# Performance work log

Measured on AMD Instinct MI355X. Metric: run time of the kernel, lower is better.

The kernel has to match this reference:

```python
import jax, jax.numpy as jnp
import numpy as np

B, H, T, D = 4, 16, 1024, 64
M = H * D  # model_dim = 1024
P = 2 * T - 1  # relative position length


def rel_shift(x):
    # x: (B, H, T, 2T-1) -> (B, H, T, T)
    b, h, t1, p = x.shape
    zero_pad = jnp.zeros((b, h, t1, 1), dtype=x.dtype)
    x_padded = jnp.concatenate([zero_pad, x], axis=-1)        # (B,H,T,2T)
    x_padded = x_padded.reshape(b, h, p + 1, t1)              # (B,H,2T,T)
    x = x_padded[:, :, 1:].reshape(b, h, t1, p)               # (B,H,T,2T-1)
    return x[:, :, :, : p // 2 + 1]                           # (B,H,T,T)


def setup_inputs() -> dict:
    key = jax.random.key(0)
    ks = jax.random.split(key, 7)
    q = jax.random.normal(ks[0], (B, H, T, D), dtype=jnp.float32)
    k = jax.random.normal(ks[1], (B, H, T, D), dtype=jnp.float32)
    v = jax.random.normal(ks[2], (B, H, T, D), dtype=jnp.float32)
    pos_emb = jax.random.normal(ks[3], (1, P, M), dtype=jnp.float32)
    attention_mask = jnp.ones((B, 1, 1, T), dtype=bool)
    # learned params
    W_pos = jax.random.normal(ks[4], (M, M), dtype=jnp.float32) * (M ** -0.5)
    pos_bias_u = jax.random.normal(ks[5], (H, D), dtype=jnp.float32) * 0.02
    pos_bias_v = jax.random.normal(ks[6], (H, D), dtype=jnp.float32) * 0.02
    return {"q": q, "k": k, "v": v, "pos_emb": pos_emb,
            "attention_mask": attention_mask, "W_pos": W_pos,
            "pos_bias_u": pos_bias_u, "pos_bias_v": pos_bias_v}


def reference(q, k, v, pos_emb, attention_mask, W_pos, pos_bias_u, pos_bias_v):
    # q, k, v: (B, H, T, D); pos_emb: (1, P, M)
    q_u = q + pos_bias_u[None, :, None, :]
    q_v = q + pos_bias_v[None, :, None, :]
    # linear_pos (no bias), split heads: (1, H, P, D)
    p = (pos_emb @ W_pos.T).reshape(pos_emb.shape[0], -1, H, D).transpose(0, 2, 1, 3)
    matrix_ac = jnp.einsum('bhqd,bhkd->bhqk', q_u, k)          # (B,H,T,T)
    matrix_bd = jnp.einsum('bhqd,hpd->bhqp', q_v, p[0])        # (B,H,T,P)
    matrix_bd = rel_shift(matrix_bd)                           # (B,H,T,T)
    scale = q.shape[-1] ** -0.5
    sim = (matrix_ac + matrix_bd) * scale
    sim = jnp.where(attention_mask, sim, jnp.finfo(sim.dtype).min)
    attn = jax.nn.softmax(sim, axis=-1)
    return jnp.einsum('bhqk,bhkd->bhqd', attn, v)
```

## Files before the change

### kernel.cpp

```cpp
#include <hip/hip_runtime.h>
#include <hip/hip_bf16.h>

#define BB 4
#define HH 16
#define TT 1024
#define DD 64
#define PP 2047
#define MM 1024

typedef __bf16 bf16;
typedef __bf16 bf16x8 __attribute__((ext_vector_type(8)));
typedef float  f32x4  __attribute__((ext_vector_type(4)));

__device__ inline bf16x8 pack8(float4 a, float4 b) {
    bf16x8 r;
    r[0]=(bf16)a.x; r[1]=(bf16)a.y; r[2]=(bf16)a.z; r[3]=(bf16)a.w;
    r[4]=(bf16)b.x; r[5]=(bf16)b.y; r[6]=(bf16)b.z; r[7]=(bf16)b.w;
    return r;
}

__device__ inline bf16x8 pack8_add_scale(float4 a, float4 b, float4 c, float4 d, float s) {
    bf16x8 r;
    r[0]=(bf16)((a.x+c.x)*s); r[1]=(bf16)((a.y+c.y)*s); r[2]=(bf16)((a.z+c.z)*s); r[3]=(bf16)((a.w+c.w)*s);
    r[4]=(bf16)((b.x+d.x)*s); r[5]=(bf16)((b.y+d.y)*s); r[6]=(bf16)((b.z+d.z)*s); r[7]=(bf16)((b.w+d.w)*s);
    return r;
}

__device__ inline unsigned pk2(float a, float b) {
    union { __bf16 h[2]; unsigned u; } x;
    x.h[0] = (__bf16)a; x.h[1] = (__bf16)b;
    return x.u;
}
__device__ inline float lo2f(unsigned u) { return __uint_as_float(u << 16); }
__device__ inline float hi2f(unsigned u) { return __uint_as_float(u & 0xffff0000u); }

__global__ __launch_bounds__(256) void prep_kv_kernel(const float* __restrict__ k,
                                                      const float* __restrict__ v,
                                                      bf16* __restrict__ k_bf,
                                                      bf16* __restrict__ vt) {
    __shared__ __attribute__((aligned(16))) bf16 Tld[64][72];
    const int t = threadIdx.x;
    const int bh = blockIdx.y;
    const int t0 = blockIdx.x * 64;
    const int r = t >> 2, c0 = (t & 3) * 16;
    {
        const float4* src = (const float4*)(k + ((size_t)bh * TT + t0 + r) * DD + c0);
        float4 a = src[0], b = src[1], c = src[2], d = src[3];
        bf16* dst = k_bf + ((size_t)bh * TT + t0 + r) * DD + c0;
        *(bf16x8*)dst       = pack8(a, b);
        *(bf16x8*)(dst + 8) = pack8(c, d);
    }
    {
        const float4* src = (const float4*)(v + ((size_t)bh * TT + t0 + r) * DD + c0);
        float4 a = src[0], b = src[1], c = src[2], d = src[3];
        *(bf16x8*)&Tld[r][c0]     = pack8(a, b);
        *(bf16x8*)&Tld[r][c0 + 8] = pack8(c, d);
    }
    __syncthreads();
    const int dd = t >> 2, j0l = (t & 3) * 16;
    bf16x8 o0, o1;
#pragma unroll
    for (int i = 0; i < 8; ++i) o0[i] = Tld[j0l + i][dd];
#pragma unroll
    for (int i = 0; i < 8; ++i) o1[i] = Tld[j0l + 8 + i][dd];
    bf16* dst = vt + ((size_t)bh * DD + dd) * TT + t0 + j0l;
    *(bf16x8*)dst = o0;
    *(bf16x8*)(dst + 8) = o1;
}

__global__ __launch_bounds__(256) void pos_gemm_kernel(const float* __restrict__ pos_emb,
                                                       const float* __restrict__ W_pos,
                                                       bf16* __restrict__ p_bf) {
    __shared__ __attribute__((aligned(16))) bf16 Abuf[64][72];
    __shared__ __attribute__((aligned(16))) bf16 Bbuf[128][72];
    const int t = threadIdx.x;
    const int w = t >> 6, lane = t & 63, quad = lane >> 4, col = lane & 15;
    const int wr = w >> 1, wc = w & 1;
    const int pp0 = blockIdx.x * 64;
    const int n0 = blockIdx.y * 128;

    f32x4 acc[2][4];
#pragma unroll
    for (int i = 0; i < 2; ++i)
#pragma unroll
        for (int j = 0; j < 4; ++j) acc[i][j] = (f32x4){0.f,0.f,0.f,0.f};

    for (int kt = 0; kt < 16; ++kt) {
        const int k0 = kt * 64;
        __syncthreads();
        {
            const int row = t >> 2, ch = (t & 3) * 16;
            const int pp = pp0 + row;
            if (pp < PP) {
                const float4* s = (const float4*)(pos_emb + (size_t)pp * MM + k0 + ch);
                float4 a = s[0], b = s[1], c = s[2], d = s[3];
                *(bf16x8*)&Abuf[row][ch]     = pack8(a, b);
                *(bf16x8*)&Abuf[row][ch + 8] = pack8(c, d);
            } else {
                float4 z = make_float4(0.f,0.f,0.f,0.f);
                *(bf16x8*)&Abuf[row][ch]     = pack8(z, z);
                *(bf16x8*)&Abuf[row][ch + 8] = pack8(z, z);
            }
        }
#pragma unroll
        for (int c = 0; c < 2; ++c) {
            const int idx = t * 2 + c;
            const int row = idx >> 2, ch = (idx & 3) * 16;
            const float4* s = (const float4*)(W_pos + (size_t)(n0 + row) * MM + k0 + ch);
            float4 a = s[0], b = s[1], cc = s[2], d = s[3];
            *(bf16x8*)&Bbuf[row][ch]     = pack8(a, b);
            *(bf16x8*)&Bbuf[row][ch + 8] = pack8(cc, d);
        }
        __syncthreads();
#pragma unroll
        for (int mt = 0; mt < 2; ++mt) {
            const int ar = wr * 32 + mt * 16 + col;
            const bf16x8 a0 = *(const bf16x8*)&Abuf[ar][quad * 8];
            const bf16x8 a1 = *(const bf16x8*)&Abuf[ar][32 + quad * 8];
#pragma unroll
            for (int nt = 0; nt < 4; ++nt) {
                const int br = wc * 64 + nt * 16 + col;
                const bf16x8 b0 = *(const bf16x8*)&Bbuf[br][quad * 8];
                const bf16x8 b1 = *(const bf16x8*)&Bbuf[br][32 + quad * 8];
                acc[mt][nt] = __builtin_amdgcn_mfma_f32_16x16x32_bf16(a0, b0, acc[mt][nt], 0, 0, 0);
                acc[mt][nt] = __builtin_amdgcn_mfma_f32_16x16x32_bf16(a1, b1, acc[mt][nt], 0, 0, 0);
            }
        }
    }
#pragma unroll
    for (int mt = 0; mt < 2; ++mt)
#pragma unroll
        for (int nt = 0; nt < 4; ++nt)
#pragma unroll
            for (int reg = 0; reg < 4; ++reg) {
                const int pp = pp0 + wr * 32 + mt * 16 + quad * 4 + reg;
                if (pp < PP) {
                    const int n = n0 + wc * 64 + nt * 16 + col;
                    p_bf[((size_t)(n >> 6) * PP + pp) * DD + (n & 63)] = (bf16)acc[mt][nt][reg];
                }
            }
}

__global__ __launch_bounds__(256, 3) void flash_kernel(const float* __restrict__ q,
                                                       const bf16* __restrict__ k_bf,
                                                       const bf16* __restrict__ vt_g,
                                                       const bf16* __restrict__ p_bf,
                                                       const float* __restrict__ bias_u,
                                                       const float* __restrict__ bias_v,
                                                       float* __restrict__ out) {
    __shared__ __attribute__((aligned(16))) bf16 Kld[64][72];
    __shared__ __attribute__((aligned(16))) bf16 Vt[64][72];
    __shared__ __attribute__((aligned(16))) bf16 Sp[4][16][72];
    __shared__ __attribute__((aligned(16))) bf16 Pring[128][72];

    const int t = threadIdx.x;
    const int w = t >> 6, lane = t & 63, quad = lane >> 4, col = lane & 15;
    const int id = blockIdx.x;
    const int bh = (id & 7) | (((id >> 3) & 7) << 3);
    const int i0 = (id >> 6) * 64;
    const int h = bh & 15;
    const int rq = i0 + 16 * w;

    const float c1 = 0.18033688011112042f;

    bf16x8 qu[2], qv[2];
    {
        const float* qrow = q + ((size_t)bh * TT + rq + col) * DD;
        const float* urow = bias_u + h * DD;
        const float* vrow = bias_v + h * DD;
#pragma unroll
        for (int kk = 0; kk < 2; ++kk) {
            const int off = kk * 32 + quad * 8;
            float4 f0 = *(const float4*)(qrow + off);
            float4 f1 = *(const float4*)(qrow + off + 4);
            float4 u0 = *(const float4*)(urow + off);
            float4 u1 = *(const float4*)(urow + off + 4);
            float4 v0 = *(const float4*)(vrow + off);
            float4 v1 = *(const float4*)(vrow + off + 4);
            qu[kk] = pack8_add_scale(f0, f1, u0, u1, c1);
            qv[kk] = pack8_add_scale(f0, f1, v0, v1, c1);
        }
    }

    f32x4 acc[4];
#pragma unroll
    for (int jt = 0; jt < 4; ++jt) acc[jt] = (f32x4){0.f,0.f,0.f,0.f};
    float lpart[4] = {0.f, 0.f, 0.f, 0.f};

    const size_t kvb = (size_t)bh * TT;
#pragma unroll
    for (int c = 0; c < 2; ++c) {
        const int idx = c * 256 + t;
        const int row = idx >> 3, ch = (idx & 7) * 8;
        *(bf16x8*)&Kld[row][ch] = *(const bf16x8*)(k_bf + (kvb + row) * DD + ch);
        *(bf16x8*)&Vt[row][ch]  = *(const bf16x8*)(vt_g + ((size_t)bh * DD + row) * TT + ch);
    }
    const int pmin0 = 960 - i0;
#pragma unroll
    for (int c = 0; c < 4; ++c) {
        const int idx = c * 256 + t;
        const int row = idx >> 3, ch = (idx & 7) * 8;
        const int pp = pmin0 + row;
        *(bf16x8*)&Pring[pp & 127][ch] =
            *(const bf16x8*)(p_bf + ((size_t)h * PP + pp) * DD + ch);
    }
    __syncthreads();

    for (int j0 = 0; j0 < TT; j0 += 64) {
        const bool has_next = (j0 + 64 < TT);

        bf16x8 kst[2], vst[2], pst[2];
        if (has_next) {
#pragma unroll
            for (int c = 0; c < 2; ++c) {
                const int idx = c * 256 + t;
                const int row = idx >> 3, ch = (idx & 7) * 8;
                kst[c] = *(const bf16x8*)(k_bf + (kvb + j0 + 64 + row) * DD + ch);
                vst[c] = *(const bf16x8*)(vt_g + ((size_t)bh * DD + row) * TT + j0 + 64 + ch);
                const int pp = 1088 + j0 - i0 + row;
                pst[c] = *(const bf16x8*)(p_bf + ((size_t)h * PP + pp) * DD + ch);
            }
        }

        __builtin_amdgcn_s_setprio(1);
        f32x4 s[4];
#pragma unroll
        for (int jt = 0; jt < 4; ++jt) {
            bf16x8 kb0 = *(const bf16x8*)&Kld[jt * 16 + col][quad * 8];
            bf16x8 kb1 = *(const bf16x8*)&Kld[jt * 16 + col][32 + quad * 8];
            f32x4 z0 = {0.f,0.f,0.f,0.f};
            z0 = __builtin_amdgcn_mfma_f32_16x16x32_bf16(qu[0], kb0, z0, 0, 0, 0);
            z0 = __builtin_amdgcn_mfma_f32_16x16x32_bf16(qu[1], kb1, z0, 0, 0, 0);
            s[jt] = z0;
        }

        const int fbw = j0 - rq + 1008;
        f32x4 z[5];
#pragma unroll
        for (int g = 0; g < 5; ++g) {
            const int phys = (fbw + 16 * g + col) & 127;
            bf16x8 pb0 = *(const bf16x8*)&Pring[phys][quad * 8];
            bf16x8 pb1 = *(const bf16x8*)&Pring[phys][32 + quad * 8];
            f32x4 zz = {0.f,0.f,0.f,0.f};
            zz = __builtin_amdgcn_mfma_f32_16x16x32_bf16(qv[0], pb0, zz, 0, 0, 0);
            zz = __builtin_amdgcn_mfma_f32_16x16x32_bf16(qv[1], pb1, zz, 0, 0, 0);
            z[g] = zz;
        }
        __builtin_amdgcn_s_setprio(0);

#pragma unroll
        for (int reg = 0; reg < 4; ++reg) {
            const int rl = quad * 4 + reg;
            const int sc2 = (col + 15 - rl) & 15;
            const int idx2 = ((lane & 48) | sc2) << 2;
            unsigned pm[4];
#pragma unroll
            for (int jt = 0; jt < 4; ++jt)
                pm[jt] = (unsigned)__builtin_amdgcn_ds_bpermute(
                    idx2, (int)pk2(z[jt][reg], z[jt + 1][reg]));
            const bool low = (col <= rl);
#pragma unroll
            for (int jt = 0; jt < 4; ++jt) {
                const float bd = low ? lo2f(pm[jt]) : hi2f(pm[jt]);
                const float pv = exp2f(s[jt][reg] + bd);
                lpart[reg] += pv;
                s[jt][reg] = pv;
            }
        }

#pragma unroll
        for (int reg = 0; reg < 4; ++reg) {
            const int rl = quad * 4 + reg;
            const int dsw = 16 * ((rl >> 3) & 1);
#pragma unroll
            for (int jt = 0; jt < 4; ++jt)
                Sp[w][rl][(jt * 16 + col + dsw) & 63] = (bf16)s[jt][reg];
        }
        const int rsw = 16 * ((col >> 3) & 1);
        __builtin_amdgcn_s_setprio(1);
#pragma unroll
        for (int kk = 0; kk < 2; ++kk) {
            bf16x8 af = *(const bf16x8*)&Sp[w][col][(kk * 32 + quad * 8 + rsw) & 63];
#pragma unroll
            for (int jt = 0; jt < 4; ++jt) {
                bf16x8 vb = *(const bf16x8*)&Vt[jt * 16 + col][kk * 32 + quad * 8];
                acc[jt] = __builtin_amdgcn_mfma_f32_16x16x32_bf16(af, vb, acc[jt], 0, 0, 0);
            }
        }
        __builtin_amdgcn_s_setprio(0);

        if (has_next) {
            __syncthreads();
#pragma unroll
            for (int c = 0; c < 2; ++c) {
                const int idx = c * 256 + t;
                const int row = idx >> 3, ch = (idx & 7) * 8;
                *(bf16x8*)&Kld[row][ch] = kst[c];
                *(bf16x8*)&Vt[row][ch]  = vst[c];
                const int ppu = 1088 + j0 - i0 + row;
                *(bf16x8*)&Pring[ppu & 127][ch] = pst[c];
            }
            __syncthreads();
        }
    }

#pragma unroll
    for (int reg = 0; reg < 4; ++reg) {
        float lt = lpart[reg];
#pragma unroll
        for (int off = 1; off < 16; off <<= 1) lt += __shfl_xor(lt, off, 64);
        const float inv = 1.0f / lt;
        const int rg = rq + quad * 4 + reg;
#pragma unroll
        for (int jt = 0; jt < 4; ++jt)
            out[((size_t)bh * TT + rg) * DD + jt * 16 + col] = acc[jt][reg] * inv;
    }
}

extern "C" void kernel_launch(void* const* d_in, const int* in_sizes, int n_in,
                              void* d_out, int out_size, void* d_ws, size_t ws_size,
                              hipStream_t stream) {
    const float* q       = (const float*)d_in[0];
    const float* k       = (const float*)d_in[1];
    const float* v       = (const float*)d_in[2];
    const float* pos_emb = (const float*)d_in[3];
    const float* W_pos   = (const float*)d_in[5];
    const float* bias_u  = (const float*)d_in[6];
    const float* bias_v  = (const float*)d_in[7];
    float* out = (float*)d_out;

    char* ws = (char*)d_ws;
    bf16* k_bf = (bf16*)(ws);
    bf16* vt_g = (bf16*)(ws + 8388608);
    bf16* p_bf = (bf16*)(ws + 16777216);

    prep_kv_kernel<<<dim3(16, 64), 256, 0, stream>>>(k, v, k_bf, vt_g);
    pos_gemm_kernel<<<dim3(32, 8), 256, 0, stream>>>(pos_emb, W_pos, p_bf);
    flash_kernel<<<1024, 256, 0, stream>>>(q, k_bf, vt_g, p_bf, bias_u, bias_v, out);
}
```

Before: 211.8 us.

## Register-prefetch pos GEMM tiles, shrink its N tile, make flash prefetch unconditional

The pos-embedding GEMM now loads the next K-slice into registers before the MFMA work on the current shared tile, then writes it to shared memory afterwards. Its N tile shrinks from 128 to 64 columns, doubling the grid so more blocks run on the GPU. In the flash kernel the next K/V/P tile loads lose their has_next branch and use clamped indices, with a sched_barrier so the loads are issued ahead of the compute. This adds redundant loads and an extra shared-memory write round on the last iteration.

```diff
diff --git a/kernel.cpp b/kernel.cpp
--- a/kernel.cpp
+++ b/kernel.cpp
@@ -72,70 +72,75 @@
                                                        const float* __restrict__ W_pos,
                                                        bf16* __restrict__ p_bf) {
     __shared__ __attribute__((aligned(16))) bf16 Abuf[64][72];
-    __shared__ __attribute__((aligned(16))) bf16 Bbuf[128][72];
+    __shared__ __attribute__((aligned(16))) bf16 Bbuf[64][72];
     const int t = threadIdx.x;
     const int w = t >> 6, lane = t & 63, quad = lane >> 4, col = lane & 15;
     const int wr = w >> 1, wc = w & 1;
     const int pp0 = blockIdx.x * 64;
-    const int n0 = blockIdx.y * 128;
-
-    f32x4 acc[2][4];
+    const int n0 = blockIdx.y * 64;
+    const int row = t >> 2, c0 = (t & 3) * 16;
+
+    const float* Arow = pos_emb + (size_t)min(pp0 + row, PP - 1) * MM + c0;
+    const float* Brow = W_pos + (size_t)(n0 + row) * MM + c0;
+
+    f32x4 acc[2][2];
 #pragma unroll
     for (int i = 0; i < 2; ++i)
 #pragma unroll
-        for (int j = 0; j < 4; ++j) acc[i][j] = (f32x4){0.f,0.f,0.f,0.f};
+        for (int j = 0; j < 2; ++j) acc[i][j] = (f32x4){0.f,0.f,0.f,0.f};
+
+    {
+        float4 a0 = *(const float4*)(Arow),     a1 = *(const float4*)(Arow + 4);
+        float4 a2 = *(const float4*)(Arow + 8), a3 = *(const float4*)(Arow + 12);
+        float4 b0 = *(const float4*)(Brow),     b1 = *(const float4*)(Brow + 4);
+        float4 b2 = *(const float4*)(Brow + 8), b3 = *(const float4*)(Brow + 12);
+        *(bf16x8*)&Abuf[row][c0]     = pack8(a0, a1);
+        *(bf16x8*)&Abuf[row][c0 + 8] = pack8(a2, a3);
+        *(bf16x8*)&Bbuf[row][c0]     = pack8(b0, b1);
+        *(bf16x8*)&Bbuf[row][c0 + 8] = pack8(b2, b3);
+    }
+    __syncthreads();
 
     for (int kt = 0; kt < 16; ++kt) {
-        const int k0 = kt * 64;
-        __syncthreads();
-        {
-            const int row = t >> 2, ch = (t & 3) * 16;
-            const int pp = pp0 + row;
-            if (pp < PP) {
-                const float4* s = (const float4*)(pos_emb + (size_t)pp * MM + k0 + ch);
-                float4 a = s[0], b = s[1], c = s[2], d = s[3];
-                *(bf16x8*)&Abuf[row][ch]     = pack8(a, b);
-                *(bf16x8*)&Abuf[row][ch + 8] = pack8(c, d);
-            } else {
-                float4 z = make_float4(0.f,0.f,0.f,0.f);
-                *(bf16x8*)&Abuf[row][ch]     = pack8(z, z);
-                *(bf16x8*)&Abuf[row][ch + 8] = pack8(z, z);
-            }
-        }
-#pragma unroll
-        for (int c = 0; c < 2; ++c) {
-            const int idx = t * 2 + c;
-            const int row = idx >> 2, ch = (idx & 3) * 16;
-            const float4* s = (const float4*)(W_pos + (size_t)(n0 + row) * MM + k0 + ch);
-            float4 a = s[0], b = s[1], cc = s[2], d = s[3];
-            *(bf16x8*)&Bbuf[row][ch]     = pack8(a, b);
-            *(bf16x8*)&Bbuf[row][ch + 8] = pack8(cc, d);
-        }
-        __syncthreads();
+        const int kc = min(kt + 1, 15) * 64;
+        float4 a0 = *(const float4*)(Arow + kc),     a1 = *(const float4*)(Arow + kc + 4);
+        float4 a2 = *(const float4*)(Arow + kc + 8), a3 = *(const float4*)(Arow + kc + 12);
+        float4 b0 = *(const float4*)(Brow + kc),     b1 = *(const float4*)(Brow + kc + 4);
+        float4 b2 = *(const float4*)(Brow + kc + 8), b3 = *(const float4*)(Brow + kc + 12);
+        __builtin_amdgcn_sched_barrier(0);
+
 #pragma unroll
         for (int mt = 0; mt < 2; ++mt) {
             const int ar = wr * 32 + mt * 16 + col;
-            const bf16x8 a0 = *(const bf16x8*)&Abuf[ar][quad * 8];
-            const bf16x8 a1 = *(const bf16x8*)&Abuf[ar][32 + quad * 8];
-#pragma unroll
-            for (int nt = 0; nt < 4; ++nt) {
-                const int br = wc * 64 + nt * 16 + col;
-                const bf16x8 b0 = *(const bf16x8*)&Bbuf[br][quad * 8];
-                const bf16x8 b1 = *(const bf16x8*)&Bbuf[br][32 + quad * 8];
-                acc[mt][nt] = __builtin_amdgcn_mfma_f32_16x16x32_bf16(a0, b0, acc[mt][nt], 0, 0, 0);
-                acc[mt][nt] = __builtin_amdgcn_mfma_f32_16x16x32_bf16(a1, b1, acc[mt][nt], 0, 0, 0);
+            const bf16x8 fa0 = *(const bf16x8*)&Abuf[ar][quad * 8];
+            const bf16x8 fa1 = *(const bf16x8*)&Abuf[ar][32 + quad * 8];
+#pragma unroll
+            for (int nt = 0; nt < 2; ++nt) {
+                const int br = wc * 32 + nt * 16 + col;
+                const bf16x8 fb0 = *(const bf16x8*)&Bbuf[br][quad * 8];
+                const bf16x8 fb1 = *(const bf16x8*)&Bbuf[br][32 + quad * 8];
+                acc[mt][nt] = __builtin_amdgcn_mfma_f32_16x16x32_bf16(fa0, fb0, acc[mt][nt], 0, 0, 0);
+                acc[mt][nt] = __builtin_amdgcn_mfma_f32_16x16x32_bf16(fa1, fb1, acc[mt][nt], 0, 0, 0);
             }
         }
-    }
+
+        __syncthreads();
+        *(bf16x8*)&Abuf[row][c0]     = pack8(a0, a1);
+        *(bf16x8*)&Abuf[row][c0 + 8] = pack8(a2, a3);
+        *(bf16x8*)&Bbuf[row][c0]     = pack8(b0, b1);
+        *(bf16x8*)&Bbuf[row][c0 + 8] = pack8(b2, b3);
+        __syncthreads();
+    }
+
 #pragma unroll
     for (int mt = 0; mt < 2; ++mt)
 #pragma unroll
-        for (int nt = 0; nt < 4; ++nt)
+        for (int nt = 0; nt < 2; ++nt)
 #pragma unroll
             for (int reg = 0; reg < 4; ++reg) {
                 const int pp = pp0 + wr * 32 + mt * 16 + quad * 4 + reg;
                 if (pp < PP) {
-                    const int n = n0 + wc * 64 + nt * 16 + col;
+                    const int n = n0 + wc * 32 + nt * 16 + col;
                     p_bf[((size_t)(n >> 6) * PP + pp) * DD + (n & 63)] = (bf16)acc[mt][nt][reg];
                 }
             }
@@ -207,20 +212,18 @@
     __syncthreads();
 
     for (int j0 = 0; j0 < TT; j0 += 64) {
-        const bool has_next = (j0 + 64 < TT);
-
         bf16x8 kst[2], vst[2], pst[2];
-        if (has_next) {
-#pragma unroll
-            for (int c = 0; c < 2; ++c) {
-                const int idx = c * 256 + t;
-                const int row = idx >> 3, ch = (idx & 7) * 8;
-                kst[c] = *(const bf16x8*)(k_bf + (kvb + j0 + 64 + row) * DD + ch);
-                vst[c] = *(const bf16x8*)(vt_g + ((size_t)bh * DD + row) * TT + j0 + 64 + ch);
-                const int pp = 1088 + j0 - i0 + row;
-                pst[c] = *(const bf16x8*)(p_bf + ((size_t)h * PP + pp) * DD + ch);
-            }
-        }
+        const int jc = min(j0 + 64, TT - 64);
+#pragma unroll
+        for (int c = 0; c < 2; ++c) {
+            const int idx = c * 256 + t;
+            const int row = idx >> 3, ch = (idx & 7) * 8;
+            kst[c] = *(const bf16x8*)(k_bf + (kvb + jc + row) * DD + ch);
+            vst[c] = *(const bf16x8*)(vt_g + ((size_t)bh * DD + row) * TT + jc + ch);
+            const int pp = min(1088 + j0 - i0 + row, PP - 1);
+            pst[c] = *(const bf16x8*)(p_bf + ((size_t)h * PP + pp) * DD + ch);
+        }
+        __builtin_amdgcn_sched_barrier(0);
 
         __builtin_amdgcn_s_setprio(1);
         f32x4 s[4];
@@ -289,19 +292,17 @@
         }
         __builtin_amdgcn_s_setprio(0);
 
-        if (has_next) {
-            __syncthreads();
-#pragma unroll
-            for (int c = 0; c < 2; ++c) {
-                const int idx = c * 256 + t;
-                const int row = idx >> 3, ch = (idx & 7) * 8;
-                *(bf16x8*)&Kld[row][ch] = kst[c];
-                *(bf16x8*)&Vt[row][ch]  = vst[c];
-                const int ppu = 1088 + j0 - i0 + row;
-                *(bf16x8*)&Pring[ppu & 127][ch] = pst[c];
-            }
-            __syncthreads();
-        }
+        __syncthreads();
+#pragma unroll
+        for (int c = 0; c < 2; ++c) {
+            const int idx = c * 256 + t;
+            const int row = idx >> 3, ch = (idx & 7) * 8;
+            *(bf16x8*)&Kld[row][ch] = kst[c];
+            *(bf16x8*)&Vt[row][ch]  = vst[c];
+            const int ppu = 1088 + j0 - i0 + row;
+            *(bf16x8*)&Pring[ppu & 127][ch] = pst[c];
+        }
+        __syncthreads();
     }
 
 #pragma unroll
@@ -335,6 +336,6 @@
     bf16* p_bf = (bf16*)(ws + 16777216);
 
     prep_kv_kernel<<<dim3(16, 64), 256, 0, stream>>>(k, v, k_bf, vt_g);
-    pos_gemm_kernel<<<dim3(32, 8), 256, 0, stream>>>(pos_emb, W_pos, p_bf);
+    pos_gemm_kernel<<<dim3(32, 16), 256, 0, stream>>>(pos_emb, W_pos, p_bf);
     flash_kernel<<<1024, 256, 0, stream>>>(q, k_bf, vt_g, p_bf, bias_u, bias_v, out);
 }
```

Result: faster. 199.4 us (-5.9%).
